# Optimization experiments

Hardware: AMD Instinct MI355X
Metric: run time of the kernel (lower is better)

The kernel has to match this reference:

```python
import jax, jax.numpy as jnp
import numpy as np

NEG_SLOPE = 0.2
EPS = 1e-08


def conv3d_same(x, w, b):
    # x: [b,c,d,h,w], w: [o,c,kd,kh,kw], stride 1, pad SAME (==pad 1 for k=3)
    y = jax.lax.conv_general_dilated(x, w, (1, 1, 1), 'SAME',
                                     dimension_numbers=('NCDHW', 'OIDHW', 'NCDHW'))
    return y + b[None, :, None, None, None]


def get_bl(frame):
    # frame: [b,3,h,w]; replicates numpy median/mean/std stats from get_BL
    x = jnp.clip(frame, 0.0, 1.0) * 255.0
    bsz = x.shape[0]
    r_med = jnp.median(x[:, 0].reshape(bsz, -1), axis=1)          # [b]
    g_mean = jnp.mean(x[:, 1], axis=(1, 2))
    g_std = jnp.std(x[:, 1], axis=(1, 2))                          # ddof=0, like np.std
    b_mean = jnp.mean(x[:, 2], axis=(1, 2))
    b_std = jnp.std(x[:, 2], axis=(1, 2))
    bl_r = 140.0 / (1.0 + 14.4 * jnp.exp(-0.034 * r_med))
    bl_g = 1.13 * g_mean + 1.11 * g_std - 25.6
    bl_b = 1.13 * b_mean + 1.11 * b_std - 25.6
    bl = jnp.stack([bl_r, bl_g, bl_b], axis=1)                     # [b,3]
    bl = jnp.clip(bl, 5.0, 250.0) / 255.0
    h, w = frame.shape[2], frame.shape[3]
    return jnp.broadcast_to(bl[:, :, None, None], (bsz, 3, h, w))


def leaky(x):
    return jnp.where(x >= 0, x, NEG_SLOPE * x)


def reference(i, j, w_bl1, b_bl1, w_bl2, b_bl2, w_t1, b_t1, w_t2, b_t2, w1, w2, t_bias):
    T = i.shape[2]
    # background light from the center frame (detached in the original)
    bl2d = jax.lax.stop_gradient(get_bl(i[:, :, T // 2]))          # [b,3,h,w]
    bl = jnp.broadcast_to(bl2d[:, :, None], i.shape)               # [b,3,T,h,w]
    j5 = jnp.broadcast_to(j[:, :, None], i.shape)                  # [b,3,T,h,w]
    # AdaptiveAvgPool3d((T,1,1)) == mean over h,w keeping frames
    diff = jnp.mean(i - j5, axis=(3, 4), keepdims=True)            # [b,3,T,1,1]
    # bl_ca: two 1x1x1 convs == channel-mixing matmuls
    h1 = leaky(jnp.einsum('bcdhw,oc->bodhw', diff, w_bl1[:, :, 0, 0, 0])
               + b_bl1[None, :, None, None, None])
    bl_diff = jax.nn.sigmoid(jnp.einsum('bcdhw,oc->bodhw', h1, w_bl2[:, :, 0, 0, 0])
                             + b_bl2[None, :, None, None, None])   # [b,3,T,1,1]
    bl = bl + w1 * bl_diff                                         # broadcast over h,w
    t3 = (i - bl) / (j5 - bl + EPS)
    x = i + w2 * t3
    h2 = leaky(conv3d_same(x, w_t1, b_t1))                         # [b,16,T,h,w]
    t = jax.nn.sigmoid(conv3d_same(h2, w_t2, b_t2)) + t_bias       # [b,1,T,h,w]
    return bl, t


def setup_inputs() -> dict:
    key = jax.random.key(0)
    ks = jax.random.split(key, 12)
    b, c, T, h, w = 4, 3, 5, 512, 512
    nf = 16
    inp = {
        'i': jax.random.uniform(ks[0], (b, c, T, h, w), dtype=jnp.float32),
        'j': jax.random.uniform(ks[1], (b, c, h, w), dtype=jnp.float32),
        'w_bl1': jax.random.normal(ks[2], (nf, 3, 1, 1, 1), dtype=jnp.float32) * 0.1,
        'b_bl1': jnp.zeros((nf,), jnp.float32),
        'w_bl2': jax.random.normal(ks[3], (3, nf, 1, 1, 1), dtype=jnp.float32) * 0.1,
        'b_bl2': jnp.zeros((3,), jnp.float32),
        'w_t1': jax.random.normal(ks[4], (nf, 3, 3, 3, 3), dtype=jnp.float32) * 0.1,
        'b_t1': jnp.zeros((nf,), jnp.float32),
        'w_t2': jax.random.normal(ks[5], (1, nf, 3, 3, 3), dtype=jnp.float32) * 0.1,
        'b_t2': jnp.zeros((1,), jnp.float32),
        'w1': jnp.zeros((1,), jnp.float32),
        'w2': jnp.zeros((1,), jnp.float32),
        't_bias': jnp.zeros((1, 1, T, 1, 1), jnp.float32),
    }
    return inp
```

## Files before the change

kernel.cpp:

```cpp
#include <hip/hip_runtime.h>

typedef unsigned int uint;
typedef unsigned short ushort;
typedef short bf16x8 __attribute__((ext_vector_type(8)));
typedef _Float16 f16x8 __attribute__((ext_vector_type(8)));
typedef float f32x4 __attribute__((ext_vector_type(4)));

#define NEG_SLOPE 0.2f

#define WS_HIST 0
#define WS_DBL  65536
#define WS_BLV  (WS_DBL + 704)
#define WS_WA   (WS_BLV + 256)
#define WS_W2A  (WS_WA + 4096)
#define WS_ZERO_BYTES (WS_DBL + 704)

#define HCH 28
#define HROW 504

__device__ __forceinline__ float leakyf(float x) { return fmaxf(x, NEG_SLOPE * x); }

__device__ __forceinline__ ushort f2bf(float f) {
  uint u = __float_as_uint(f);
  uint r = u + 0x7FFFu + ((u >> 16) & 1u);
  return (ushort)(r >> 16);
}
__device__ __forceinline__ uint cvt_pk_u32(float a, float b) {
  union { __fp16 __attribute__((ext_vector_type(2))) h; uint u; } c;
  c.h = __builtin_amdgcn_cvt_pkrtz(a, b);
  return c.u;
}

__global__ __launch_bounds__(256) void stats_kernel(const float* __restrict__ gi,
                                                    const float* __restrict__ gj,
                                                    double* __restrict__ sums,
                                                    uint* __restrict__ hist) {
  __shared__ double red[256];
  __shared__ uint lh[4096];
  const int plane = blockIdx.y;
  const int chunk = blockIdx.x;
  const int tid = threadIdx.x;

  if (plane >= 60) {
    const int jp = plane - 60;
    const float4* base = (const float4*)(gj + (size_t)jp * 262144);
    double dsum = 0.0;
    for (int k = 0; k < 8; ++k) {
      float4 v = base[chunk * 2048 + k * 256 + tid];
      dsum += (double)v.x + (double)v.y + (double)v.z + (double)v.w;
    }
    red[tid] = dsum; __syncthreads();
    for (int off = 128; off > 0; off >>= 1) { if (tid < off) red[tid] += red[tid + off]; __syncthreads(); }
    if (tid == 0) atomicAdd(&sums[60 + jp], red[0]);
    return;
  }

  const int b = plane / 15;
  const int rem = plane % 15;
  const int c = rem / 5;
  const int t = rem % 5;
  const float4* base = (const float4*)(gi + (size_t)plane * 262144);
  const bool dostat = (c >= 1 && t == 2);
  const bool domed = (c == 0 && t == 2);
  if (domed) {
    for (int i = tid; i < 4096; i += 256) lh[i] = 0;
    __syncthreads();
  }
  double dsum = 0.0, dsx = 0.0, dsx2 = 0.0;
  for (int k = 0; k < 8; ++k) {
    float4 v = base[chunk * 2048 + k * 256 + tid];
    dsum += (double)v.x + (double)v.y + (double)v.z + (double)v.w;
    if (dostat || domed) {
      float arr[4] = {v.x, v.y, v.z, v.w};
#pragma unroll
      for (int q = 0; q < 4; ++q) {
        float x = fminf(fmaxf(arr[q], 0.f), 1.f) * 255.f;
        if (domed) {
          int bin = (int)(x * (4096.0f / 255.0f));
          if (bin > 4095) bin = 4095;
          atomicAdd(&lh[bin], 1u);
        } else {
          dsx += (double)x;
          dsx2 += (double)x * (double)x;
        }
      }
    }
  }
  red[tid] = dsum; __syncthreads();
  for (int off = 128; off > 0; off >>= 1) { if (tid < off) red[tid] += red[tid + off]; __syncthreads(); }
  if (tid == 0) atomicAdd(&sums[plane], red[0]);
  __syncthreads();
  if (dostat) {
    red[tid] = dsx; __syncthreads();
    for (int off = 128; off > 0; off >>= 1) { if (tid < off) red[tid] += red[tid + off]; __syncthreads(); }
    if (tid == 0) atomicAdd(&sums[72 + b * 2 + (c - 1)], red[0]);
    __syncthreads();
    red[tid] = dsx2; __syncthreads();
    for (int off = 128; off > 0; off >>= 1) { if (tid < off) red[tid] += red[tid + off]; __syncthreads(); }
    if (tid == 0) atomicAdd(&sums[80 + b * 2 + (c - 1)], red[0]);
  }
  if (domed) {
    for (int i = tid; i < 4096; i += 256) { uint v = lh[i]; if (v) atomicAdd(&hist[b * 4096 + i], v); }
  }
}

__global__ void setup_kernel(const float* __restrict__ w_t1, const float* __restrict__ w_t2,
                             ushort* __restrict__ wA, ushort* __restrict__ w2A) {
  const int tid = threadIdx.x;
  for (int idx = tid; idx < 2048; idx += 256) {
    int o = idx >> 7, k = idx & 127, g = k >> 2, kw = k & 3;
    float v = 0.f;
    if (g < 27 && kw < 3) {
      int ci = g / 9, kd = (g % 9) / 3, kh = g % 3;
      v = w_t1[o * 81 + ci * 27 + kd * 9 + kh * 3 + kw];
    }
    wA[idx] = f2bf(v);
  }
  for (int idx = tid; idx < 12800; idx += 256) {
    int j = idx & 7;
    int lane = (idx >> 3) & 63;
    int rest = idx >> 9;
    int step = rest % 5;
    int tf = rest / 5;
    int ln = lane & 15, kb = lane >> 4;
    int k = kb * 8 + j;
    int tap = step * 2 + (k >> 4);
    int ch = k & 15;
    float v = 0.f;
    if (ln < 5 && tap < 9) {
      int kd = tf + 1 - ln;
      if (kd >= 0 && kd <= 2) v = w_t2[ch * 27 + kd * 9 + tap];
    }
    union { ushort s; _Float16 h; } cv; cv.h = (_Float16)v;
    w2A[idx] = cv.s;
  }
}

__global__ __launch_bounds__(256) void finalize_kernel(const uint* __restrict__ hist,
                                const double* __restrict__ sums,
                                const float* __restrict__ w_bl1, const float* __restrict__ b_bl1,
                                const float* __restrict__ w_bl2, const float* __restrict__ b_bl2,
                                const float* __restrict__ w1, float* __restrict__ blv) {
  __shared__ uint s[256];
  __shared__ float fv[2];
  __shared__ float rmed_s[4];
  const int tid = threadIdx.x;
  for (int b = 0; b < 4; ++b) {
    const uint* h = hist + b * 4096;
    uint loc[16]; uint part = 0;
#pragma unroll
    for (int q = 0; q < 16; ++q) { loc[q] = h[tid * 16 + q]; part += loc[q]; }
    s[tid] = part; __syncthreads();
    for (int off = 1; off < 256; off <<= 1) {
      uint v = (tid >= off) ? s[tid - off] : 0u;
      __syncthreads(); s[tid] += v; __syncthreads();
    }
    uint pref = s[tid] - part;
#pragma unroll
    for (int m = 0; m < 2; ++m) {
      uint k = 131071u + (uint)m;
      if (k >= pref && k < pref + part) {
        uint cum = pref;
        for (int q = 0; q < 16; ++q) {
          if (k < cum + loc[q]) { fv[m] = ((float)(tid * 16 + q) + 0.5f) * (255.f / 4096.f); break; }
          cum += loc[q];
        }
      }
    }
    __syncthreads();
    if (tid == 0) rmed_s[b] = 0.5f * (fv[0] + fv[1]);
    __syncthreads();
  }
  if (tid < 20) {
    const int b = tid / 5, t = tid % 5;
    const double inv = 1.0 / 262144.0;
    float bl2[3];
    bl2[0] = 140.f / (1.f + 14.4f * expf(-0.034f * rmed_s[b]));
    for (int c = 1; c < 3; ++c) {
      double m = sums[72 + b * 2 + (c - 1)] * inv;
      double ex2 = sums[80 + b * 2 + (c - 1)] * inv;
      double var = ex2 - m * m;
      if (var < 0.0) var = 0.0;
      bl2[c] = (float)(1.13 * m + 1.11 * sqrt(var) - 25.6);
    }
#pragma unroll
    for (int c = 0; c < 3; ++c)
      bl2[c] = fminf(fmaxf(bl2[c], 5.f), 250.f) * (1.f / 255.f);
    float diff[3];
    for (int c = 0; c < 3; ++c)
      diff[c] = (float)((sums[(b * 3 + c) * 5 + t] - sums[60 + b * 3 + c]) * inv);
    float h1[16];
    for (int o = 0; o < 16; ++o) {
      float sv = b_bl1[o];
      for (int c = 0; c < 3; ++c) sv += w_bl1[o * 3 + c] * diff[c];
      h1[o] = leakyf(sv);
    }
    const float w1v = w1[0];
    for (int c = 0; c < 3; ++c) {
      float sv = b_bl2[c];
      for (int o = 0; o < 16; ++o) sv += w_bl2[c * 16 + o] * h1[o];
      float sg = 1.f / (1.f + expf(-sv));
      blv[(b * 3 + c) * 5 + t] = bl2[c] + w1v * sg;
    }
  }
}

__global__ __launch_bounds__(256, 3) void fused_kernel(
    const float* __restrict__ gi, const float* __restrict__ gj,
    const ushort* __restrict__ wAg, const float* __restrict__ b_t1,
    const ushort* __restrict__ w2Ag, const float* __restrict__ b_t2,
    const float* __restrict__ w2p, const float* __restrict__ t_bias,
    const float* __restrict__ blv, float* __restrict__ out) {
  __shared__ __align__(16) ushort xsh[10560];
  __shared__ __align__(16) ushort h2sh[324 * HCH];
  __shared__ __align__(16) int baseTab[160];
  __shared__ float blv_s[15];

  const int b = blockIdx.z;
  const int lin = blockIdx.y * 32 + blockIdx.x;
  const int swz = (lin & 7) * 128 + (lin >> 3);
  const int tY = swz >> 5, tX = swz & 31;
  const int tid = threadIdx.x;
  const int wv = tid >> 6;
  const int lane = tid & 63;
  const int ln = lane & 15;
  const int kb = lane >> 4;
  const int ty = tid >> 4, tx = tid & 15;
  const int gy = tY * 16 + ty, gx = tX * 16 + tx;
  const int ybase = tY * 16 - 2, xbase = tX * 16 - 2;

  if (tid < 15) blv_s[tid] = blv[b * 15 + tid];
  for (int i = tid; i < 5280; i += 256) ((uint*)xsh)[i] = 0u;
  if (tid < 160) {
    int tf_ = tid >> 5, kb_ = (tid >> 3) & 3, e = tid & 7;
    int g = (e >> 1) * 8 + kb_ * 2 + (e & 1);
    int sl = 3, sb = 0;
    if (g < 27) {
      int ci = g / 9, r9 = g % 9, kd = r9 / 3, kh = r9 % 3;
      sb = ci * 440 + kh * 22;
      int f = tf_ + kd - 1;
      if (f >= 0 && f <= 4) sl = f % 3;
    }
    baseTab[tid] = sb + sl * 1320;
  }

  union { uint4 u; bf16x8 v; } a4[4];
#pragma unroll
  for (int m = 0; m < 4; ++m)
    a4[m].u = *(const uint4*)(wAg + ln * 128 + m * 32 + kb * 8);
  f32x4 bias4;
#pragma unroll
  for (int r = 0; r < 4; ++r) bias4[r] = b_t1[kb * 4 + r];

  int pT[6];
  uint tmask = 0;
#pragma unroll
  for (int i = 0; i < 6; ++i) {
    int tile = wv + i * 4;
    int pos = tile * 16 + ln;
    int pe = pos < 324 ? pos : 323;
    int y0 = pe / 18, x0 = pe - y0 * 18;
    int p = x0 & 1;
    pT[i] = (y0 * 22 + x0 - p + p * 5280) | (pe << 13);
    int gyh = tY * 16 - 1 + y0, gxh = tX * 16 - 1 + x0;
    if (pos < 324) tmask |= 1u << i;
    if (gyh >= 0 && gyh < 512 && gxh >= 0 && gxh < 512) tmask |= 1u << (i + 8);
  }

  int bOff[5];
#pragma unroll
  for (int s = 0; s < 5; ++s) {
    int tap = s * 2 + (kb >> 1); if (tap > 8) tap = 8;
    int kh = tap / 3, kw = tap - kh * 3;
    bOff[s] = kh * HROW + kw * HCH + (kb & 1) * 8 + ln * HCH;
  }

  int qi5[5], eb5[5];
  uint civpack = 0;
  float jv5[5];
  uint vmask = 0;
#pragma unroll
  for (int k = 0; k < 5; ++k) {
    int idx = tid + k * 256;
    int idc = idx < 1200 ? idx : 0;
    int ci = idc / 400, rem = idc - ci * 400;
    int ys = rem / 20, xx = rem - ys * 20;
    int gyy = ybase + ys, gxx = xbase + xx;
    bool inb = (idx < 1200) && gyy >= 0 && gyy < 512 && gxx >= 0 && gxx < 512;
    int cy = gyy < 0 ? 0 : (gyy > 511 ? 511 : gyy);
    int cx = gxx < 0 ? 0 : (gxx > 511 ? 511 : gxx);
    int spc = cy * 512 + cx;
    qi5[k] = (b * 3 + ci) * 1310720 + spc;
    jv5[k] = gj[(b * 3 + ci) * 262144 + spc];
    eb5[k] = ci * 440 + ys * 22 + xx;
    civpack |= (uint)(ci * 5) << (k * 4);
    if (inb) vmask |= 1u << k;
    if (xx > 0) vmask |= 1u << (k + 8);
  }

  const float w2v = w2p[0];

  auto issue_loads = [&](int f, float* ivr) {
    const int fo = f * 262144;
    ivr[0] = gi[qi5[0] + fo];
    ivr[1] = gi[qi5[1] + fo];
    ivr[2] = gi[qi5[2] + fo];
    ivr[3] = gi[qi5[3] + fo];
    ivr[4] = (tid < 176) ? gi[qi5[4] + fo] : 0.f;
  };
  auto stage_frame = [&](int f, const float* ivr) {
    const int slot = f % 3;
    const int sb2 = slot * 1320;
#pragma unroll
    for (int k = 0; k < 5; ++k) {
      if (k == 4 && tid >= 176) break;
      float iv = ivr[k];
      float bv = blv_s[((civpack >> (k * 4)) & 15u) + f];
      float num = iv - bv;
      float den = jv5[k] - bv + 1e-8f;
      float xv = ((vmask >> k) & 1u) ? fmaf(w2v, num * __builtin_amdgcn_rcpf(den), iv) : 0.f;
      ushort hx = f2bf(xv);
      int ebb = sb2 + eb5[k];
      xsh[ebb] = hx;
      if ((vmask >> (k + 8)) & 1u) xsh[ebb + 5279] = hx;
    }
  };

  float ivr0[5], ivr1[5];
  issue_loads(0, ivr0);
  issue_loads(1, ivr1);

  __syncthreads();

#pragma unroll
  for (int c = 0; c < 3; ++c)
#pragma unroll
    for (int t = 0; t < 5; ++t)
      out[(((b * 3 + c) * 5 + t) * 512 + gy) * 512 + gx] = blv_s[c * 5 + t];

  stage_frame(0, ivr0);
  stage_frame(1, ivr1);
  __syncthreads();

  f32x4 acc2[4];
#pragma unroll
  for (int u = 0; u < 4; ++u) acc2[u] = (f32x4){0.f, 0.f, 0.f, 0.f};

#pragma unroll
  for (int tf = 0; tf < 5; ++tf) {
    float ivr[5];
    if (tf < 3) issue_loads(tf + 2, ivr);

    union { uint4 u; f16x8 v; } aw[5];
#pragma unroll
    for (int s = 0; s < 5; ++s)
      aw[s].u = *(const uint4*)(w2Ag + ((tf * 5 + s) * 64 + lane) * 8);

    int4 bE0 = *(const int4*)&baseTab[tf * 32 + kb * 8];
    int4 bE1 = *(const int4*)&baseTab[tf * 32 + kb * 8 + 4];

#pragma unroll
    for (int i = 0; i < 6; ++i) {
      if (i == 5 && wv != 0) continue;
      const int pT_ = pT[i];
      const int q = pT_ & 8191;
      f32x4 acc = bias4;
#pragma unroll
      for (int m = 0; m < 4; ++m) {
        int be0 = (m == 0) ? bE0.x : (m == 1) ? bE0.z : (m == 2) ? bE1.x : bE1.z;
        int be1 = (m == 0) ? bE0.y : (m == 1) ? bE0.w : (m == 2) ? bE1.y : bE1.w;
        const uint* p0 = (const uint*)(xsh + (be0 + q));
        const uint* p1 = (const uint*)(xsh + (be1 + q));
        union { uint4 u; bf16x8 v; } bfr;
        bfr.u = make_uint4(p0[0], p0[1], p1[0], p1[1]);
        acc = __builtin_amdgcn_mfma_f32_16x16x32_bf16(a4[m].v, bfr.v, acc, 0, 0, 0);
      }
      const bool inimg = (tmask >> (i + 8)) & 1u;
      float r0 = inimg ? leakyf(acc[0]) : 0.f;
      float r1 = inimg ? leakyf(acc[1]) : 0.f;
      float r2 = inimg ? leakyf(acc[2]) : 0.f;
      float r3 = inimg ? leakyf(acc[3]) : 0.f;
      uint p0 = cvt_pk_u32(r0, r1);
      uint p1 = cvt_pk_u32(r2, r3);
      if ((tmask >> i) & 1u)
        *(uint2*)(h2sh + ((pT_ >> 13) * HCH + kb * 4)) = make_uint2(p0, p1);
    }
    __syncthreads();

#pragma unroll
    for (int u = 0; u < 4; ++u) {
      const int tt = wv + u * 4;
      const ushort* hb = h2sh + tt * HROW;
#pragma unroll
      for (int s = 0; s < 5; ++s) {
        uint2 lo = *(const uint2*)(hb + bOff[s]);
        uint2 hi = *(const uint2*)(hb + bOff[s] + 4);
        union { uint4 u4; f16x8 v; } bfr;
        bfr.u4 = make_uint4(lo.x, lo.y, hi.x, hi.y);
        acc2[u] = __builtin_amdgcn_mfma_f32_16x16x32_f16(aw[s].v, bfr.v, acc2[u], 0, 0, 0);
      }
    }

    if (tf < 3) stage_frame(tf + 2, ivr);
    __syncthreads();
  }

  float* sredf = (float*)xsh;
#pragma unroll
  for (int u = 0; u < 4; ++u) {
    const int tt = wv + u * 4;
    if (kb == 0) {
#pragma unroll
      for (int r = 0; r < 4; ++r)
        sredf[r * 256 + tt * 16 + ln] = acc2[u][r];
    } else if (kb == 1) {
      sredf[4 * 256 + tt * 16 + ln] = acc2[u][0];
    }
  }
  __syncthreads();

  const float bt2 = b_t2[0];
#pragma unroll
  for (int t = 0; t < 5; ++t) {
    float tv = 1.f / (1.f + __expf(-(sredf[t * 256 + tid] + bt2))) + t_bias[t];
    out[15728640 + ((b * 5 + t) * 512 + gy) * 512 + gx] = tv;
  }
}

extern "C" void kernel_launch(void* const* d_in, const int* in_sizes, int n_in,
                              void* d_out, int out_size, void* d_ws, size_t ws_size,
                              hipStream_t stream) {
  const float* gi = (const float*)d_in[0];
  const float* gj = (const float*)d_in[1];
  const float* w_bl1 = (const float*)d_in[2];
  const float* b_bl1 = (const float*)d_in[3];
  const float* w_bl2 = (const float*)d_in[4];
  const float* b_bl2 = (const float*)d_in[5];
  const float* w_t1 = (const float*)d_in[6];
  const float* b_t1 = (const float*)d_in[7];
  const float* w_t2 = (const float*)d_in[8];
  const float* b_t2 = (const float*)d_in[9];
  const float* w1 = (const float*)d_in[10];
  const float* w2 = (const float*)d_in[11];
  const float* t_bias = (const float*)d_in[12];
  float* out = (float*)d_out;
  char* ws = (char*)d_ws;

  uint* hist = (uint*)(ws + WS_HIST);
  double* sums = (double*)(ws + WS_DBL);
  float* blv = (float*)(ws + WS_BLV);
  ushort* wA = (ushort*)(ws + WS_WA);
  ushort* w2A = (ushort*)(ws + WS_W2A);

  hipMemsetAsync(ws, 0, WS_ZERO_BYTES, stream);

  setup_kernel<<<1, 256, 0, stream>>>(w_t1, w_t2, wA, w2A);
  stats_kernel<<<dim3(32, 72), 256, 0, stream>>>(gi, gj, sums, hist);
  finalize_kernel<<<1, 256, 0, stream>>>(hist, sums, w_bl1, b_bl1, w_bl2, b_bl2, w1, blv);
  fused_kernel<<<dim3(32, 32, 4), 256, 0, stream>>>(gi, gj, wA, b_t1, w2A, b_t2, w2, t_bias, blv, out);
}
```

Baseline: 151.5 us.

## Double-buffer conv2 h2 staging to remove one barrier per frame

Splits the h2 shared buffer into two ping-pong halves, each with a narrower channel stride, so the second conv for frame tf-1 runs in the same phase as the first conv for frame tf. This drops one __syncthreads per frame iteration and lets the two MFMA streams interleave. The x staging ring changes from three slots indexed mod 3 to slots indexed f&3, and slot 1 is explicitly zeroed so the boundary frame reads padding. In exchange, shared memory grows and the bOff, HCH and halo indexing must stay consistent, otherwise results or occupancy could suffer.

```diff
diff --git a/kernel.cpp b/kernel.cpp
--- a/kernel.cpp
+++ b/kernel.cpp
@@ -15,8 +15,9 @@
 #define WS_W2A  (WS_WA + 4096)
 #define WS_ZERO_BYTES (WS_DBL + 704)
 
-#define HCH 28
-#define HROW 504
+#define HCH 24
+#define HROW 432
+#define HBUF 7776
 
 __device__ __forceinline__ float leakyf(float x) { return fmaxf(x, NEG_SLOPE * x); }
 
@@ -212,7 +213,7 @@
     const float* __restrict__ w2p, const float* __restrict__ t_bias,
     const float* __restrict__ blv, float* __restrict__ out) {
   __shared__ __align__(16) ushort xsh[10560];
-  __shared__ __align__(16) ushort h2sh[324 * HCH];
+  __shared__ __align__(16) ushort h2sh[2 * HBUF];
   __shared__ __align__(16) int baseTab[160];
   __shared__ float blv_s[15];
 
@@ -239,7 +240,7 @@
       int ci = g / 9, r9 = g % 9, kd = r9 / 3, kh = r9 % 3;
       sb = ci * 440 + kh * 22;
       int f = tf_ + kd - 1;
-      if (f >= 0 && f <= 4) sl = f % 3;
+      sl = (f < 0) ? 3 : (f > 4) ? 1 : (f & 3);
     }
     baseTab[tid] = sb + sl * 1320;
   }
@@ -309,8 +310,7 @@
     ivr[4] = (tid < 176) ? gi[qi5[4] + fo] : 0.f;
   };
   auto stage_frame = [&](int f, const float* ivr) {
-    const int slot = f % 3;
-    const int sb2 = slot * 1320;
+    const int sb2 = (f & 3) * 1320;
 #pragma unroll
     for (int k = 0; k < 5; ++k) {
       if (k == 4 && tid >= 176) break;
@@ -325,6 +325,16 @@
       if ((vmask >> (k + 8)) & 1u) xsh[ebb + 5279] = hx;
     }
   };
+  auto stage_zero = [&](int slot) {
+    const int sb2 = slot * 1320;
+#pragma unroll
+    for (int k = 0; k < 5; ++k) {
+      if (k == 4 && tid >= 176) break;
+      int ebb = sb2 + eb5[k];
+      xsh[ebb] = 0;
+      if ((vmask >> (k + 8)) & 1u) xsh[ebb + 5279] = 0;
+    }
+  };
 
   float ivr0[5], ivr1[5];
   issue_loads(0, ivr0);
@@ -352,13 +362,16 @@
     if (tf < 3) issue_loads(tf + 2, ivr);
 
     union { uint4 u; f16x8 v; } aw[5];
-#pragma unroll
-    for (int s = 0; s < 5; ++s)
-      aw[s].u = *(const uint4*)(w2Ag + ((tf * 5 + s) * 64 + lane) * 8);
+    if (tf > 0) {
+#pragma unroll
+      for (int s = 0; s < 5; ++s)
+        aw[s].u = *(const uint4*)(w2Ag + (((tf - 1) * 5 + s) * 64 + lane) * 8);
+    }
 
     int4 bE0 = *(const int4*)&baseTab[tf * 32 + kb * 8];
     int4 bE1 = *(const int4*)&baseTab[tf * 32 + kb * 8 + 4];
 
+    ushort* h2w = h2sh + (tf & 1) * HBUF;
 #pragma unroll
     for (int i = 0; i < 6; ++i) {
       if (i == 5 && wv != 0) continue;
@@ -383,14 +396,41 @@
       uint p0 = cvt_pk_u32(r0, r1);
       uint p1 = cvt_pk_u32(r2, r3);
       if ((tmask >> i) & 1u)
-        *(uint2*)(h2sh + ((pT_ >> 13) * HCH + kb * 4)) = make_uint2(p0, p1);
-    }
+        *(uint2*)(h2w + ((pT_ >> 13) * HCH + kb * 4)) = make_uint2(p0, p1);
+    }
+
+    if (tf > 0) {
+      const ushort* h2r = h2sh + ((tf - 1) & 1) * HBUF;
+#pragma unroll
+      for (int u = 0; u < 4; ++u) {
+        const int tt = wv + u * 4;
+        const ushort* hb = h2r + tt * HROW;
+#pragma unroll
+        for (int s = 0; s < 5; ++s) {
+          uint2 lo = *(const uint2*)(hb + bOff[s]);
+          uint2 hi = *(const uint2*)(hb + bOff[s] + 4);
+          union { uint4 u4; f16x8 v; } bfr;
+          bfr.u4 = make_uint4(lo.x, lo.y, hi.x, hi.y);
+          acc2[u] = __builtin_amdgcn_mfma_f32_16x16x32_f16(aw[s].v, bfr.v, acc2[u], 0, 0, 0);
+        }
+      }
+    }
+
+    if (tf < 3) stage_frame(tf + 2, ivr);
+    else if (tf == 3) stage_zero(1);
     __syncthreads();
-
+  }
+
+  {
+    union { uint4 u; f16x8 v; } aw[5];
+#pragma unroll
+    for (int s = 0; s < 5; ++s)
+      aw[s].u = *(const uint4*)(w2Ag + ((4 * 5 + s) * 64 + lane) * 8);
+    const ushort* h2r = h2sh + 0 * HBUF;
 #pragma unroll
     for (int u = 0; u < 4; ++u) {
       const int tt = wv + u * 4;
-      const ushort* hb = h2sh + tt * HROW;
+      const ushort* hb = h2r + tt * HROW;
 #pragma unroll
       for (int s = 0; s < 5; ++s) {
         uint2 lo = *(const uint2*)(hb + bOff[s]);
@@ -400,9 +440,6 @@
         acc2[u] = __builtin_amdgcn_mfma_f32_16x16x32_f16(aw[s].v, bfr.v, acc2[u], 0, 0, 0);
       }
     }
-
-    if (tf < 3) stage_frame(tf + 2, ivr);
-    __syncthreads();
   }
 
   float* sredf = (float*)xsh;
```

Measured after the change: 152.0 us. No clear change (+0.3%).
